# Performance work log

Measured on AMD Instinct MI355X. Metric: run time of the kernel, lower is better.

The kernel has to match this reference:

```python
import jax, jax.numpy as jnp
import numpy as np

BN_EPS = 1e-5
R = 8.0        # radius
L = 11         # sequence kernel size (odd), s = L//2
K = 24         # kernel_channels[-1]
N_NODES = 32768
N_EDGES = 524288
C_IN = 128     # in_channels == out_channels
C_W = 32       # width = out_channels * base_width / 64


def _bn(x, gamma, beta):
    # BatchNorm1d in training mode: biased batch statistics over node dim
    mu = jnp.mean(x, axis=0)
    var = jnp.mean(jnp.square(x - mu), axis=0)
    return (x - mu) * jax.lax.rsqrt(var + BN_EPS) * gamma + beta


def _lrelu(x, slope):
    return jnp.where(x >= 0, x, slope * x)


def setup_inputs() -> dict:
    key = jax.random.key(0)
    ks = jax.random.split(key, 10)

    def glorot(k, shape, fan_in):
        return jax.random.normal(k, shape, jnp.float32) * np.float32(1.0 / np.sqrt(fan_in))

    inp = {}
    inp["x"] = jax.random.normal(ks[0], (N_NODES, C_IN), jnp.float32)
    inp["pos"] = jax.random.normal(ks[1], (N_NODES, 3), jnp.float32) * 10.0
    inp["ori"] = jax.random.normal(ks[2], (N_NODES, 9), jnp.float32)
    inp["seq"] = jnp.arange(N_NODES, dtype=jnp.int32)
    inp["edge_index"] = jax.random.randint(ks[3], (2, N_EDGES), 0, N_NODES, jnp.int32)
    # input MLP params: BN(C_IN) -> LeakyReLU(0.1) -> Linear(C_IN->C_W, no bias) -> BN(C_W) -> LeakyReLU(0.1)
    inp["bn1_g"] = jnp.ones((C_IN,), jnp.float32)
    inp["bn1_b"] = jnp.zeros((C_IN,), jnp.float32)
    inp["lin1_w"] = glorot(ks[4], (C_IN, C_W), C_IN)
    inp["bn2_g"] = jnp.ones((C_W,), jnp.float32)
    inp["bn2_b"] = jnp.zeros((C_W,), jnp.float32)
    # CDConv WeightNet (single layer kernel_channels=[K]): per-seq-bin affine 7 -> K
    inp["wn_w"] = glorot(ks[5], (L, 7, K), 7)
    inp["wn_b"] = jnp.zeros((L, K), jnp.float32)
    # CDConv output projection: [K*C_W, C_W]
    inp["conv_w"] = glorot(ks[6], (K * C_W, C_W), K * C_W)
    # output Linear: BN(C_W) -> LeakyReLU(0.1) -> Linear(C_W->C_IN, no bias)
    inp["bn3_g"] = jnp.ones((C_W,), jnp.float32)
    inp["bn3_b"] = jnp.zeros((C_W,), jnp.float32)
    inp["lin2_w"] = glorot(ks[7], (C_W, C_IN), C_W)
    return inp


def reference(x, pos, ori, seq, edge_index,
              bn1_g, bn1_b, lin1_w, bn2_g, bn2_b,
              wn_w, wn_b, conv_w, bn3_g, bn3_b, lin2_w):
    n = x.shape[0]
    identity = x  # in_channels == out_channels -> identity branch is passthrough

    # ----- input MLP (mid_channels=None) -----
    h = _lrelu(_bn(x, bn1_g, bn1_b), 0.1)
    h = h @ lin1_w                       # [N, C_W]
    h = _lrelu(_bn(h, bn2_g, bn2_b), 0.1)

    # ----- CDConv: continuous geometric kernel over neighbor edges -----
    src, dst = edge_index[0], edge_index[1]      # message j=src -> i=dst
    d = pos[src] - pos[dst]                      # [E,3]
    dist = jnp.linalg.norm(d, axis=-1, keepdims=True)
    direction = d / (dist + 1e-9)
    Ri = ori[dst].reshape(-1, 3, 3)              # receiver local frame
    Rj = ori[src].reshape(-1, 3, 3)
    pos_local = jnp.einsum('eij,ej->ei', Ri, direction)      # direction in local frame
    ori_feat = jnp.einsum('eij,ej->ei', Ri, Rj[:, 0, :])     # neighbor axis in local frame
    delta = jnp.concatenate([pos_local, ori_feat, dist / R], axis=-1)  # [E,7]

    s = L // 2
    sidx = jnp.clip(seq[src] - seq[dst], -s, s) + s          # [E] in [0, L)

    # WeightNet: per-edge affine selected by sequence bin, LeakyReLU(0.2)
    w = _lrelu(jnp.einsum('ef,efk->ek', delta, wn_w[sidx]) + wn_b[sidx], 0.2)  # [E,K]

    # message = outer(kernel_weight, x_j), scatter-sum to receivers
    msg = (w[:, :, None] * h[src][:, None, :]).reshape(w.shape[0], K * C_W)   # [E, K*C_W]
    agg = jax.ops.segment_sum(msg, dst, num_segments=n)                        # [N, K*C_W]
    h = agg @ conv_w                                                            # [N, C_W]

    # ----- output Linear + residual -----
    h = _lrelu(_bn(h, bn3_g, bn3_b), 0.1)
    out = h @ lin2_w + identity
    return out
```

## Files before the change

### kernel.cpp

```cpp
#include <hip/hip_runtime.h>

#define N_NODES 32768
#define C_IN 128
#define C_W 32
#define KK 24
#define SS 5
#define GG 8
#define AGS (KK * C_W + 4)

#define LD6(W, PTR) do { const float4* _p = (const float4*)(PTR); \
  W[0]=_p[0]; W[1]=_p[1]; W[2]=_p[2]; W[3]=_p[3]; W[4]=_p[4]; W[5]=_p[5]; } while(0)

#define ACC24(W, V) do { float _v = (V); \
  a[0]+=W[0].x*_v;  a[1]+=W[0].y*_v;  a[2]+=W[0].z*_v;  a[3]+=W[0].w*_v;  \
  a[4]+=W[1].x*_v;  a[5]+=W[1].y*_v;  a[6]+=W[1].z*_v;  a[7]+=W[1].w*_v;  \
  a[8]+=W[2].x*_v;  a[9]+=W[2].y*_v;  a[10]+=W[2].z*_v; a[11]+=W[2].w*_v; \
  a[12]+=W[3].x*_v; a[13]+=W[3].y*_v; a[14]+=W[3].z*_v; a[15]+=W[3].w*_v; \
  a[16]+=W[4].x*_v; a[17]+=W[4].y*_v; a[18]+=W[4].z*_v; a[19]+=W[4].w*_v; \
  a[20]+=W[5].x*_v; a[21]+=W[5].y*_v; a[22]+=W[5].z*_v; a[23]+=W[5].w*_v; } while(0)

__global__ void __launch_bounds__(256) k_pre(
        const float* __restrict__ x, float* __restrict__ s1,
        const int* __restrict__ ei, int E, int* __restrict__ counts) {
    int t = threadIdx.x;
    int c = t % C_IN;
    int r0 = blockIdx.x * 2 + t / C_IN;
    float s = 0.f, sq = 0.f;
    for (int r = r0; r < N_NODES; r += 1024) {
        float v = x[(size_t)r * C_IN + c];
        s += v; sq += v * v;
    }
    atomicAdd(&s1[c], s);
    atomicAdd(&s1[C_IN + c], sq);
    for (int e = blockIdx.x * 256 + t; e < E; e += 512 * 256)
        atomicAdd(&counts[ei[E + e]], 1);
}

__global__ void __launch_bounds__(256) k_mlp1(
        const float* __restrict__ x, const float* __restrict__ s1,
        const float* __restrict__ g1, const float* __restrict__ b1,
        const float* __restrict__ w1, float* __restrict__ hpre,
        float* __restrict__ s2sh) {
    __shared__ float sAB[2][C_IN];
    __shared__ float sx[32][C_IN + 4];
    __shared__ float sw[C_IN][C_W];
    const int t = threadIdx.x;
    const int row0 = blockIdx.x * 32;
    if (t < C_IN) {
        float mean = s1[t] * (1.f / N_NODES);
        float var = s1[C_IN + t] * (1.f / N_NODES) - mean * mean;
        float a = g1[t] * rsqrtf(var + 1e-5f);
        sAB[0][t] = a; sAB[1][t] = b1[t] - mean * a;
    }
    for (int idx = t; idx < C_IN * C_W; idx += 256)
        sw[idx / C_W][idx % C_W] = w1[idx];
    __syncthreads();
    for (int idx = t; idx < 32 * 32; idx += 256) {
        int r = idx >> 5, cq = idx & 31;
        float4 v = *(const float4*)&x[(size_t)(row0 + r) * C_IN + cq * 4];
        float* d = &sx[r][cq * 4];
        float a0 = sAB[0][cq*4+0]*v.x + sAB[1][cq*4+0];
        float a1 = sAB[0][cq*4+1]*v.y + sAB[1][cq*4+1];
        float a2 = sAB[0][cq*4+2]*v.z + sAB[1][cq*4+2];
        float a3 = sAB[0][cq*4+3]*v.w + sAB[1][cq*4+3];
        d[0] = a0 >= 0.f ? a0 : 0.1f * a0;
        d[1] = a1 >= 0.f ? a1 : 0.1f * a1;
        d[2] = a2 >= 0.f ? a2 : 0.1f * a2;
        d[3] = a3 >= 0.f ? a3 : 0.1f * a3;
    }
    __syncthreads();
    const int r = t >> 3, c0 = (t & 7) * 4;
    float ac0 = 0.f, ac1 = 0.f, ac2 = 0.f, ac3 = 0.f;
    #pragma unroll 8
    for (int cc = 0; cc < C_IN; ++cc) {
        float xv = sx[r][cc];
        float4 wv = *(const float4*)&sw[cc][c0];
        ac0 += xv * wv.x; ac1 += xv * wv.y; ac2 += xv * wv.z; ac3 += xv * wv.w;
    }
    float4 o; o.x = ac0; o.y = ac1; o.z = ac2; o.w = ac3;
    *(float4*)&hpre[(size_t)(row0 + r) * C_W + c0] = o;
    __syncthreads();
    sx[r][c0] = ac0; sx[r][c0+1] = ac1; sx[r][c0+2] = ac2; sx[r][c0+3] = ac3;
    __syncthreads();
    if (t < C_W) {
        float s = 0.f, sq = 0.f;
        #pragma unroll
        for (int rr = 0; rr < 32; ++rr) {
            float v = sx[rr][t];
            s += v; sq += v * v;
        }
        int sh = (blockIdx.x & 7) * 64;
        atomicAdd(&s2sh[sh + t], s);
        atomicAdd(&s2sh[sh + C_W + t], sq);
    }
}

__global__ void __launch_bounds__(1024) k_scan(
        const int* __restrict__ counts, int* __restrict__ offsets,
        int* __restrict__ cursor) {
    __shared__ int sblk[1024];
    const int t = threadIdx.x;
    const int base = t * 32;
    const int4* cp = (const int4*)(counts + base);
    int loc[32];
    int s = 0;
    #pragma unroll
    for (int q = 0; q < 8; ++q) {
        int4 v = cp[q];
        loc[q*4+0] = s; s += v.x;
        loc[q*4+1] = s; s += v.y;
        loc[q*4+2] = s; s += v.z;
        loc[q*4+3] = s; s += v.w;
    }
    sblk[t] = s;
    __syncthreads();
    for (int d = 1; d < 1024; d <<= 1) {
        int u = (t >= d) ? sblk[t - d] : 0;
        __syncthreads();
        sblk[t] += u;
        __syncthreads();
    }
    const int blockbase = sblk[t] - s;
    #pragma unroll
    for (int q = 0; q < 8; ++q) {
        int4 o;
        o.x = blockbase + loc[q*4+0];
        o.y = blockbase + loc[q*4+1];
        o.z = blockbase + loc[q*4+2];
        o.w = blockbase + loc[q*4+3];
        ((int4*)(offsets + base))[q] = o;
        ((int4*)(cursor + base))[q] = o;
    }
    if (t == 1023) offsets[N_NODES] = sblk[1023];
}

__global__ void __launch_bounds__(256) k_edge(
        const int* __restrict__ ei, int E,
        const float* __restrict__ pos, const float* __restrict__ ori,
        const int* __restrict__ seq,
        const float* __restrict__ wnw, const float* __restrict__ wnb,
        int* __restrict__ cursor, int* __restrict__ srcPerm,
        float* __restrict__ wPerm) {
    __shared__ float sWnw[11][169];
    __shared__ float sWnb[11][24];
    const int t = threadIdx.x;
    for (int idx = t; idx < 11 * 168; idx += 256)
        sWnw[idx / 168][idx % 168] = wnw[idx];
    for (int idx = t; idx < 11 * 24; idx += 256)
        sWnb[idx / 24][idx % 24] = wnb[idx];
    __syncthreads();
    const int e = blockIdx.x * 256 + t;
    if (e >= E) return;
    const int src = ei[e];
    const int dst = ei[E + e];
    int ds = seq[src] - seq[dst];
    ds = ds < -SS ? -SS : (ds > SS ? SS : ds);
    const int sb = ds + SS;
    float dx = pos[src * 3 + 0] - pos[dst * 3 + 0];
    float dy = pos[src * 3 + 1] - pos[dst * 3 + 1];
    float dz = pos[src * 3 + 2] - pos[dst * 3 + 2];
    float dist = sqrtf(dx * dx + dy * dy + dz * dz);
    float inv = 1.f / (dist + 1e-9f);
    float ux = dx * inv, uy = dy * inv, uz = dz * inv;
    float b0 = ori[src * 9 + 0], b1 = ori[src * 9 + 1], b2 = ori[src * 9 + 2];
    float delta[7];
    #pragma unroll
    for (int r = 0; r < 3; ++r) {
        float m0 = ori[dst * 9 + r * 3 + 0];
        float m1 = ori[dst * 9 + r * 3 + 1];
        float m2 = ori[dst * 9 + r * 3 + 2];
        delta[r]     = m0 * ux + m1 * uy + m2 * uz;
        delta[3 + r] = m0 * b0 + m1 * b1 + m2 * b2;
    }
    delta[6] = dist * 0.125f;
    float w[KK];
    #pragma unroll
    for (int k = 0; k < KK; ++k) {
        float acc = sWnb[sb][k];
        #pragma unroll
        for (int f = 0; f < 7; ++f)
            acc += delta[f] * sWnw[sb][f * 24 + k];
        w[k] = acc >= 0.f ? acc : 0.2f * acc;
    }
    const int p = atomicAdd(&cursor[dst], 1);
    srcPerm[p] = src;
    float4* wp = (float4*)(wPerm + (size_t)p * KK);
    #pragma unroll
    for (int q = 0; q < 6; ++q) {
        float4 o; o.x = w[q*4]; o.y = w[q*4+1]; o.z = w[q*4+2]; o.w = w[q*4+3];
        wp[q] = o;
    }
}

__global__ void __launch_bounds__(256, 4) k_node(
    const int* __restrict__ offsets, const int* __restrict__ srcPerm,
    const float* __restrict__ wPerm, const float* __restrict__ hpre,
    const float* __restrict__ s2sh, const float* __restrict__ g2,
    const float* __restrict__ b2, const float* __restrict__ convw,
    float* __restrict__ convout, float* __restrict__ s3sh) {
    __shared__ float sA2[C_W], sB2[C_W];
    __shared__ int sOff[GG + 1];
    __shared__ float sAgg[GG][AGS];
    __shared__ float sRed[4][GG][C_W];
    __shared__ float sRv[GG][C_W], sRq[GG][C_W];
    const int i0 = blockIdx.x * GG;
    const int t = threadIdx.x;
    if (t < C_W) {
        float s = 0.f, sq = 0.f;
        #pragma unroll
        for (int j = 0; j < 8; ++j) {
            s  += s2sh[j * 64 + t];
            sq += s2sh[j * 64 + C_W + t];
        }
        float mean = s * (1.f / N_NODES);
        float var = sq * (1.f / N_NODES) - mean * mean;
        float a = g2[t] * rsqrtf(var + 1e-5f);
        sA2[t] = a; sB2[t] = b2[t] - mean * a;
    }
    if (t <= GG) sOff[t] = offsets[i0 + t];
    __syncthreads();
    const int g = t >> 5, c = t & 31;
    const float bnA = sA2[c], bnB = sB2[c];
    const int beg = sOff[g], end = sOff[g + 1];
    float a[KK];
    #pragma unroll
    for (int k = 0; k < KK; ++k) a[k] = 0.f;

    for (int cb = beg; cb < end; cb += 32) {
        const int m = min(32, end - cb);
        int srcL = (cb + c < end) ? srcPerm[cb + c] : 0;
        int j = 0;
        for (; j + 2 <= m; j += 2) {
            int s0 = __shfl(srcL, j + 0, 32);
            int s1 = __shfl(srcL, j + 1, 32);
            float h0 = hpre[(size_t)s0 * C_W + c];
            float h1 = hpre[(size_t)s1 * C_W + c];
            float4 wa[6], wb[6];
            const float* wbase = wPerm + (size_t)(cb + j) * KK;
            LD6(wa, wbase);
            LD6(wb, wbase + KK);
            float v0 = bnA * h0 + bnB; v0 = v0 >= 0.f ? v0 : 0.1f * v0;
            float v1 = bnA * h1 + bnB; v1 = v1 >= 0.f ? v1 : 0.1f * v1;
            ACC24(wa, v0);
            ACC24(wb, v1);
        }
        if (j < m) {
            int s0 = __shfl(srcL, j, 32);
            float h0 = hpre[(size_t)s0 * C_W + c];
            float4 wa[6];
            LD6(wa, wPerm + (size_t)(cb + j) * KK);
            float v0 = bnA * h0 + bnB; v0 = v0 >= 0.f ? v0 : 0.1f * v0;
            ACC24(wa, v0);
        }
    }
    #pragma unroll
    for (int k = 0; k < KK; ++k) sAgg[g][k * C_W + c] = a[k];
    __syncthreads();

    {
        const int coq = t & 7;
        const int gp  = (t >> 3) & 7;
        const int sl  = t >> 6;
        const int r0  = sl * 192;
        float4 acc; acc.x = acc.y = acc.z = acc.w = 0.f;
        #pragma unroll 4
        for (int rc = 0; rc < 192; rc += 4) {
            const float4 s4 = *(const float4*)&sAgg[gp][r0 + rc];
            const float4 w0 = *(const float4*)&convw[(size_t)(r0+rc+0)*32 + coq*4];
            const float4 w1 = *(const float4*)&convw[(size_t)(r0+rc+1)*32 + coq*4];
            const float4 w2 = *(const float4*)&convw[(size_t)(r0+rc+2)*32 + coq*4];
            const float4 w3 = *(const float4*)&convw[(size_t)(r0+rc+3)*32 + coq*4];
            acc.x += s4.x*w0.x + s4.y*w1.x + s4.z*w2.x + s4.w*w3.x;
            acc.y += s4.x*w0.y + s4.y*w1.y + s4.z*w2.y + s4.w*w3.y;
            acc.z += s4.x*w0.z + s4.y*w1.z + s4.z*w2.z + s4.w*w3.z;
            acc.w += s4.x*w0.w + s4.y*w1.w + s4.z*w2.w + s4.w*w3.w;
        }
        *(float4*)&sRed[sl][gp][coq * 4] = acc;
    }
    __syncthreads();
    {
        const int gg = t >> 5, co = t & 31;
        float v = sRed[0][gg][co] + sRed[1][gg][co] + sRed[2][gg][co] + sRed[3][gg][co];
        convout[(size_t)(i0 + gg) * C_W + co] = v;
        sRv[gg][co] = v; sRq[gg][co] = v * v;
    }
    __syncthreads();
    if (t < 64) {
        int cc = t & 31;
        bool isq = t >= C_W;
        float s = 0.f;
        #pragma unroll
        for (int gg = 0; gg < GG; ++gg)
            s += isq ? sRq[gg][cc] : sRv[gg][cc];
        atomicAdd(&s3sh[(blockIdx.x & 7) * 64 + t], s);
    }
}

__global__ void __launch_bounds__(256) k_out(
        const float* __restrict__ conv, const float* __restrict__ s3sh,
        const float* __restrict__ g3, const float* __restrict__ b3,
        const float* __restrict__ w2, const float* __restrict__ x,
        float* __restrict__ out) {
    __shared__ float sAB[2][C_W];
    __shared__ float sh[8][C_W];
    __shared__ float sw2[C_W][C_IN];
    const int t = threadIdx.x;
    const int row0 = blockIdx.x * 8;
    if (t < C_W) {
        float s = 0.f, sq = 0.f;
        #pragma unroll
        for (int j = 0; j < 8; ++j) {
            s  += s3sh[j * 64 + t];
            sq += s3sh[j * 64 + C_W + t];
        }
        float mean = s * (1.f / N_NODES);
        float var = sq * (1.f / N_NODES) - mean * mean;
        float a = g3[t] * rsqrtf(var + 1e-5f);
        sAB[0][t] = a; sAB[1][t] = b3[t] - mean * a;
    }
    for (int idx = t; idx < C_W * C_IN; idx += 256)
        sw2[idx >> 7][idx & 127] = w2[idx];
    __syncthreads();
    {
        float v = conv[(size_t)row0 * C_W + t];
        int r = t >> 5, cc = t & 31;
        v = sAB[0][cc] * v + sAB[1][cc];
        sh[r][cc] = v >= 0.f ? v : 0.1f * v;
    }
    __syncthreads();
    const int r = t >> 5, c4 = (t & 31) * 4;
    float4 acc = *(const float4*)&x[(size_t)(row0 + r) * C_IN + c4];
    #pragma unroll 8
    for (int cw = 0; cw < C_W; ++cw) {
        float hv = sh[r][cw];
        float4 wv = *(const float4*)&sw2[cw][c4];
        acc.x += hv * wv.x; acc.y += hv * wv.y;
        acc.z += hv * wv.z; acc.w += hv * wv.w;
    }
    *(float4*)&out[(size_t)(row0 + r) * C_IN + c4] = acc;
}

extern "C" void kernel_launch(void* const* d_in, const int* in_sizes, int n_in,
                              void* d_out, int out_size, void* d_ws, size_t ws_size,
                              hipStream_t stream) {
    const float* x     = (const float*)d_in[0];
    const float* pos   = (const float*)d_in[1];
    const float* ori   = (const float*)d_in[2];
    const int*   seq   = (const int*)d_in[3];
    const int*   ei    = (const int*)d_in[4];
    const float* bn1g  = (const float*)d_in[5];
    const float* bn1b  = (const float*)d_in[6];
    const float* lin1w = (const float*)d_in[7];
    const float* bn2g  = (const float*)d_in[8];
    const float* bn2b  = (const float*)d_in[9];
    const float* wnw   = (const float*)d_in[10];
    const float* wnb   = (const float*)d_in[11];
    const float* convw = (const float*)d_in[12];
    const float* bn3g  = (const float*)d_in[13];
    const float* bn3b  = (const float*)d_in[14];
    const float* lin2w = (const float*)d_in[15];
    float* out = (float*)d_out;
    const int E = in_sizes[4] / 2;

    char* wsb = (char*)d_ws;
    size_t off = 0;
    auto alloc = [&](size_t bytes) {
        void* p = wsb + off;
        off = (off + bytes + 255) & ~(size_t)255;
        return p;
    };
    float* s1      = (float*)alloc(256 * 4);
    float* s2sh    = (float*)alloc(512 * 4);
    float* s3sh    = (float*)alloc(512 * 4);
    int*   counts  = (int*)alloc((size_t)N_NODES * 4);
    size_t zero_bytes = off;
    int*   offsets = (int*)alloc(((size_t)N_NODES + 1) * 4);
    int*   cursor  = (int*)alloc((size_t)N_NODES * 4);
    int*   srcPerm = (int*)alloc((size_t)E * 4);
    float* hpre    = (float*)alloc((size_t)N_NODES * C_W * 4);
    float* convo   = (float*)alloc((size_t)N_NODES * C_W * 4);
    float* wPerm   = (float*)alloc((size_t)E * KK * 4);

    hipMemsetAsync(wsb, 0, zero_bytes, stream);

    k_pre<<<512, 256, 0, stream>>>(x, s1, ei, E, counts);
    k_scan<<<1, 1024, 0, stream>>>(counts, offsets, cursor);
    k_edge<<<(E + 255) / 256, 256, 0, stream>>>(ei, E, pos, ori, seq, wnw, wnb,
                                                cursor, srcPerm, wPerm);
    k_mlp1<<<N_NODES / 32, 256, 0, stream>>>(x, s1, bn1g, bn1b, lin1w, hpre, s2sh);
    k_node<<<N_NODES / GG, 256, 0, stream>>>(offsets, srcPerm, wPerm, hpre,
                                             s2sh, bn2g, bn2b, convw, convo, s3sh);
    k_out<<<N_NODES / 8, 256, 0, stream>>>(convo, s3sh, bn3g, bn3b, lin2w, x, out);
}
```

Before: 293.1 us.

## Use one 64-lane wave per node in k_node, staging edge weights in LDS

k_node moves from 256 to 512 threads, so each node gets a full 64-lane wavefront instead of 32 lanes. The two half-waves process alternate edges and combine their partial sums with a cross-lane xor shuffle. Each chunk of per-edge kernel weights is loaded once into shared memory with coalesced float4 loads, rather than every lane issuing redundant global loads. The conv_w projection is split over 8 slices instead of 4. The cost is more shared memory per block, which can reduce occupancy, plus an extra reduction step.

Result: faster. 275.2 us (-6.1%).

```diff
diff --git a/kernel.cpp b/kernel.cpp
--- a/kernel.cpp
+++ b/kernel.cpp
@@ -7,17 +7,6 @@
 #define SS 5
 #define GG 8
 #define AGS (KK * C_W + 4)
-
-#define LD6(W, PTR) do { const float4* _p = (const float4*)(PTR); \
-  W[0]=_p[0]; W[1]=_p[1]; W[2]=_p[2]; W[3]=_p[3]; W[4]=_p[4]; W[5]=_p[5]; } while(0)
-
-#define ACC24(W, V) do { float _v = (V); \
-  a[0]+=W[0].x*_v;  a[1]+=W[0].y*_v;  a[2]+=W[0].z*_v;  a[3]+=W[0].w*_v;  \
-  a[4]+=W[1].x*_v;  a[5]+=W[1].y*_v;  a[6]+=W[1].z*_v;  a[7]+=W[1].w*_v;  \
-  a[8]+=W[2].x*_v;  a[9]+=W[2].y*_v;  a[10]+=W[2].z*_v; a[11]+=W[2].w*_v; \
-  a[12]+=W[3].x*_v; a[13]+=W[3].y*_v; a[14]+=W[3].z*_v; a[15]+=W[3].w*_v; \
-  a[16]+=W[4].x*_v; a[17]+=W[4].y*_v; a[18]+=W[4].z*_v; a[19]+=W[4].w*_v; \
-  a[20]+=W[5].x*_v; a[21]+=W[5].y*_v; a[22]+=W[5].z*_v; a[23]+=W[5].w*_v; } while(0)
 
 __global__ void __launch_bounds__(256) k_pre(
         const float* __restrict__ x, float* __restrict__ s1,
@@ -192,7 +181,7 @@
     }
 }
 
-__global__ void __launch_bounds__(256, 4) k_node(
+__global__ void __launch_bounds__(512, 4) k_node(
     const int* __restrict__ offsets, const int* __restrict__ srcPerm,
     const float* __restrict__ wPerm, const float* __restrict__ hpre,
     const float* __restrict__ s2sh, const float* __restrict__ g2,
@@ -200,11 +189,12 @@
     float* __restrict__ convout, float* __restrict__ s3sh) {
     __shared__ float sA2[C_W], sB2[C_W];
     __shared__ int sOff[GG + 1];
+    __shared__ float sW[GG][32 * KK];
     __shared__ float sAgg[GG][AGS];
-    __shared__ float sRed[4][GG][C_W];
+    __shared__ float sRed[8][GG][C_W];
     __shared__ float sRv[GG][C_W], sRq[GG][C_W];
+    const int t = threadIdx.x;
     const int i0 = blockIdx.x * GG;
-    const int t = threadIdx.x;
     if (t < C_W) {
         float s = 0.f, sq = 0.f;
         #pragma unroll
@@ -219,52 +209,63 @@
     }
     if (t <= GG) sOff[t] = offsets[i0 + t];
     __syncthreads();
-    const int g = t >> 5, c = t & 31;
+
+    const int w    = t >> 6;
+    const int lane = t & 63;
+    const int c    = lane & 31;
+    const int s    = lane >> 5;
     const float bnA = sA2[c], bnB = sB2[c];
-    const int beg = sOff[g], end = sOff[g + 1];
+    const int beg = sOff[w], end = sOff[w + 1];
+    float* sWw = &sW[w][0];
     float a[KK];
     #pragma unroll
     for (int k = 0; k < KK; ++k) a[k] = 0.f;
 
     for (int cb = beg; cb < end; cb += 32) {
         const int m = min(32, end - cb);
-        int srcL = (cb + c < end) ? srcPerm[cb + c] : 0;
-        int j = 0;
-        for (; j + 2 <= m; j += 2) {
-            int s0 = __shfl(srcL, j + 0, 32);
-            int s1 = __shfl(srcL, j + 1, 32);
-            float h0 = hpre[(size_t)s0 * C_W + c];
-            float h1 = hpre[(size_t)s1 * C_W + c];
-            float4 wa[6], wb[6];
-            const float* wbase = wPerm + (size_t)(cb + j) * KK;
-            LD6(wa, wbase);
-            LD6(wb, wbase + KK);
-            float v0 = bnA * h0 + bnB; v0 = v0 >= 0.f ? v0 : 0.1f * v0;
-            float v1 = bnA * h1 + bnB; v1 = v1 >= 0.f ? v1 : 0.1f * v1;
-            ACC24(wa, v0);
-            ACC24(wb, v1);
-        }
-        if (j < m) {
-            int s0 = __shfl(srcL, j, 32);
-            float h0 = hpre[(size_t)s0 * C_W + c];
-            float4 wa[6];
-            LD6(wa, wPerm + (size_t)(cb + j) * KK);
-            float v0 = bnA * h0 + bnB; v0 = v0 >= 0.f ? v0 : 0.1f * v0;
-            ACC24(wa, v0);
-        }
-    }
-    #pragma unroll
-    for (int k = 0; k < KK; ++k) sAgg[g][k * C_W + c] = a[k];
+        int srcL = srcPerm[cb + min(c, m - 1)];
+        const float4* gsrc = (const float4*)(wPerm + (size_t)cb * KK);
+        #pragma unroll
+        for (int u = 0; u < 3; ++u) {
+            int idx = lane + u * 64;
+            if (idx < m * 6) ((float4*)sWw)[idx] = gsrc[idx];
+        }
+        #pragma unroll 2
+        for (int j2 = 0; j2 < m; j2 += 2) {
+            const int slot = min(j2 + s, m - 1);
+            const bool ok = (j2 + s) < m;
+            const int src = __shfl(srcL, slot, 64);
+            float h = hpre[(size_t)src * C_W + c];
+            float v = bnA * h + bnB;
+            v = v >= 0.f ? v : 0.1f * v;
+            v = ok ? v : 0.f;
+            const float4* wp = (const float4*)(sWw + slot * KK);
+            float4 W0 = wp[0], W1 = wp[1], W2 = wp[2];
+            float4 W3 = wp[3], W4 = wp[4], W5 = wp[5];
+            a[0]  += W0.x * v; a[1]  += W0.y * v; a[2]  += W0.z * v; a[3]  += W0.w * v;
+            a[4]  += W1.x * v; a[5]  += W1.y * v; a[6]  += W1.z * v; a[7]  += W1.w * v;
+            a[8]  += W2.x * v; a[9]  += W2.y * v; a[10] += W2.z * v; a[11] += W2.w * v;
+            a[12] += W3.x * v; a[13] += W3.y * v; a[14] += W3.z * v; a[15] += W3.w * v;
+            a[16] += W4.x * v; a[17] += W4.y * v; a[18] += W4.z * v; a[19] += W4.w * v;
+            a[20] += W5.x * v; a[21] += W5.y * v; a[22] += W5.z * v; a[23] += W5.w * v;
+        }
+    }
+    #pragma unroll
+    for (int k = 0; k < KK; ++k) a[k] += __shfl_xor(a[k], 32, 64);
+    if (s == 0) {
+        #pragma unroll
+        for (int k = 0; k < KK; ++k) sAgg[w][k * C_W + c] = a[k];
+    }
     __syncthreads();
 
     {
         const int coq = t & 7;
         const int gp  = (t >> 3) & 7;
-        const int sl  = t >> 6;
-        const int r0  = sl * 192;
+        const int sl8 = t >> 6;
+        const int r0  = sl8 * 96;
         float4 acc; acc.x = acc.y = acc.z = acc.w = 0.f;
-        #pragma unroll 4
-        for (int rc = 0; rc < 192; rc += 4) {
+        #pragma unroll 6
+        for (int rc = 0; rc < 96; rc += 4) {
             const float4 s4 = *(const float4*)&sAgg[gp][r0 + rc];
             const float4 w0 = *(const float4*)&convw[(size_t)(r0+rc+0)*32 + coq*4];
             const float4 w1 = *(const float4*)&convw[(size_t)(r0+rc+1)*32 + coq*4];
@@ -275,12 +276,14 @@
             acc.z += s4.x*w0.z + s4.y*w1.z + s4.z*w2.z + s4.w*w3.z;
             acc.w += s4.x*w0.w + s4.y*w1.w + s4.z*w2.w + s4.w*w3.w;
         }
-        *(float4*)&sRed[sl][gp][coq * 4] = acc;
-    }
-    __syncthreads();
-    {
+        *(float4*)&sRed[sl8][gp][coq * 4] = acc;
+    }
+    __syncthreads();
+    if (t < 256) {
         const int gg = t >> 5, co = t & 31;
-        float v = sRed[0][gg][co] + sRed[1][gg][co] + sRed[2][gg][co] + sRed[3][gg][co];
+        float v = 0.f;
+        #pragma unroll
+        for (int sl = 0; sl < 8; ++sl) v += sRed[sl][gg][co];
         convout[(size_t)(i0 + gg) * C_W + co] = v;
         sRv[gg][co] = v; sRq[gg][co] = v * v;
     }
@@ -288,11 +291,11 @@
     if (t < 64) {
         int cc = t & 31;
         bool isq = t >= C_W;
-        float s = 0.f;
+        float s2 = 0.f;
         #pragma unroll
         for (int gg = 0; gg < GG; ++gg)
-            s += isq ? sRq[gg][cc] : sRv[gg][cc];
-        atomicAdd(&s3sh[(blockIdx.x & 7) * 64 + t], s);
+            s2 += isq ? sRq[gg][cc] : sRv[gg][cc];
+        atomicAdd(&s3sh[(blockIdx.x & 7) * 64 + t], s2);
     }
 }
 
@@ -388,7 +391,7 @@
     k_edge<<<(E + 255) / 256, 256, 0, stream>>>(ei, E, pos, ori, seq, wnw, wnb,
                                                 cursor, srcPerm, wPerm);
     k_mlp1<<<N_NODES / 32, 256, 0, stream>>>(x, s1, bn1g, bn1b, lin1w, hpre, s2sh);
-    k_node<<<N_NODES / GG, 256, 0, stream>>>(offsets, srcPerm, wPerm, hpre,
+    k_node<<<N_NODES / GG, 512, 0, stream>>>(offsets, srcPerm, wPerm, hpre,
                                              s2sh, bn2g, bn2b, convw, convo, s3sh);
     k_out<<<N_NODES / 8, 256, 0, stream>>>(convo, s3sh, bn3g, bn3b, lin2w, x, out);
 }
```
